# Kernel tuning notes

Measured on AMD Instinct MI355X. Metric: run time of the kernel, lower is better.

## Reference

```python
import jax, jax.numpy as jnp
import numpy as np

B, S, E, H = 2, 2048, 512, 8
DH = E // H
SCALE = DH ** -0.5
TEMPERATURE = 1.0
LN_EPS = 1e-5


def setup_inputs() -> dict:
    key = jax.random.key(0)
    ks = jax.random.split(key, 12)
    s = E ** -0.5
    return {
        "q": jax.random.normal(ks[0], (B, S, E), jnp.float32),
        "k": jax.random.normal(ks[1], (B, S, E), jnp.float32),
        "v": jax.random.normal(ks[2], (B, S, E), jnp.float32),
        "Wq": jax.random.normal(ks[3], (E, E), jnp.float32) * s,
        "bq": jnp.zeros((E,), jnp.float32),
        "Wk": jax.random.normal(ks[4], (E, E), jnp.float32) * s,
        "bk": jnp.zeros((E,), jnp.float32),
        "Wv": jax.random.normal(ks[5], (E, E), jnp.float32) * s,
        "bv": jnp.zeros((E,), jnp.float32),
        "Wo": jax.random.normal(ks[6], (E, E), jnp.float32) * s,
        "bo": jnp.zeros((E,), jnp.float32),
        "ln_g": jnp.ones((E,), jnp.float32),
        "ln_b": jnp.zeros((E,), jnp.float32),
    }


def reference(q, k, v, Wq, bq, Wk, bk, Wv, bv, Wo, bo, ln_g, ln_b):
    # QKV projections (nn.Linear: x @ W.T + b)
    qh = (q @ Wq.T + bq).reshape(B, S, H, DH).transpose(0, 2, 1, 3)  # [B,H,S,Dh]
    kh = (k @ Wk.T + bk).reshape(B, S, H, DH).transpose(0, 2, 1, 3)
    vh = (v @ Wv.T + bv).reshape(B, S, H, DH).transpose(0, 2, 1, 3)
    # attention scores [B,H,S,S], scaled then divided by temperature
    scores = jnp.einsum('bhqd,bhkd->bhqk', qh, kh) * (SCALE / TEMPERATURE)
    attn = jax.nn.softmax(scores, axis=-1)
    # dropout is identity in eval mode
    x = jnp.einsum('bhqk,bhkd->bhqd', attn, vh)  # [B,H,S,Dh]
    x = x.transpose(0, 2, 1, 3).reshape(B, S, E)
    # out projection + LayerNorm
    y = x @ Wo.T + bo
    mu = jnp.mean(y, axis=-1, keepdims=True)
    var = jnp.var(y, axis=-1, keepdims=True)
    out = (y - mu) * jax.lax.rsqrt(var + LN_EPS) * ln_g + ln_b
    return out
```

## Files before the change

kernel.cpp:

```cpp
#include <hip/hip_runtime.h>
#include <hip/hip_bf16.h>
#include <stdint.h>

#define B_ 2
#define S_ 2048
#define E_ 512
#define H_ 8
#define DH_ 64
#define BH_ (B_*H_)
#define M_ (B_*S_)

typedef short short8 __attribute__((ext_vector_type(8)));
typedef float f32x4 __attribute__((ext_vector_type(4)));
typedef float f32x16 __attribute__((ext_vector_type(16)));
typedef int int4v __attribute__((ext_vector_type(4)));

#define QSCALE 0.18033688011112042f

#if __has_builtin(__builtin_amdgcn_exp2f)
#define EXP2(x) __builtin_amdgcn_exp2f(x)
#else
#define EXP2(x) exp2f(x)
#endif

__device__ __forceinline__ float asf(uint32_t u) { return __builtin_bit_cast(float, u); }
__device__ __forceinline__ uint32_t asu(float f) { return __builtin_bit_cast(uint32_t, f); }

__device__ __forceinline__ ushort f2bf(float f) {
  uint32_t u = __builtin_bit_cast(uint32_t, f);
  u += 0x7fffu + ((u >> 16) & 1u);
  return (ushort)(u >> 16);
}

__device__ __forceinline__ uint32_t cvtpk(float lo, float hi) {
  uint32_t r;
  asm("v_cvt_pk_bf16_f32 %0, %1, %2" : "=v"(r) : "v"(lo), "v"(hi));
  return r;
}

__device__ __forceinline__ void swap32(uint32_t a, uint32_t b, uint32_t& o0, uint32_t& o1) {
#if __has_builtin(__builtin_amdgcn_permlane32_swap)
  typedef int v2i __attribute__((ext_vector_type(2)));
  v2i r = __builtin_amdgcn_permlane32_swap((int)a, (int)b, false, false);
  o0 = (uint32_t)r.x; o1 = (uint32_t)r.y;
#else
  int laneid = (int)(threadIdx.x & 63);
  uint32_t pa = (uint32_t)__shfl_xor((int)a, 32, 64);
  uint32_t pb = (uint32_t)__shfl_xor((int)b, 32, 64);
  bool hi = laneid >= 32;
  o0 = hi ? pb : a;
  o1 = hi ? b : pa;
#endif
}

__device__ __forceinline__ void gll16(const void* g, void* l) {
  __builtin_amdgcn_global_load_lds((const __attribute__((address_space(1))) void*)g,
                                   (__attribute__((address_space(3))) void*)l,
                                   16, 0, 0);
}

struct CvtArgs {
  const float* s[7];
  ushort* d[7];
  int nq[7];
};

__global__ __launch_bounds__(256) void cvt_kernel(CvtArgs a) {
  int seg = blockIdx.y;
  int i = blockIdx.x * 256 + threadIdx.x;
  if (i >= a.nq[seg]) return;
  float4 v = ((const float4*)a.s[seg])[i];
  ushort4 o;
  o.x = f2bf(v.x); o.y = f2bf(v.y); o.z = f2bf(v.z); o.w = f2bf(v.w);
  ((ushort4*)a.d[seg])[i] = o;
}

template<int EPI>
__global__ __launch_bounds__(256) void gemm_bt(
    const ushort* __restrict__ A0, const ushort* __restrict__ A1, const ushort* __restrict__ A2,
    const ushort* __restrict__ W0, const ushort* __restrict__ W1, const ushort* __restrict__ W2,
    const float* __restrict__ bias0, const float* __restrict__ bias1, const float* __restrict__ bias2,
    ushort* O0, ushort* O1, ushort* O2, float* Yout)
{
  const int K = E_;
  int z = blockIdx.z;
  const ushort* A = (z == 0) ? A0 : ((z == 1) ? A1 : A2);
  const ushort* W = (z == 0) ? W0 : ((z == 1) ? W1 : W2);
  const float* bias = (z == 0) ? bias0 : ((z == 1) ? bias1 : bias2);
  ushort* O = (z == 0) ? O0 : ((z == 1) ? O1 : O2);
  float scale = (EPI == 0 && z == 0) ? QSCALE : 1.0f;

  int n0 = blockIdx.x * 128, m0 = blockIdx.y * 128;
  int tid = threadIdx.x, lane = tid & 63, wid = tid >> 6;
  int wm = wid >> 1, wn = wid & 1;

  __shared__ ushort As[128 * 32];
  __shared__ ushort Bs[128 * 32];

  f32x4 acc[4][4];
#pragma unroll
  for (int i = 0; i < 4; ++i)
#pragma unroll
    for (int j = 0; j < 4; ++j)
      acc[i][j] = (f32x4){0.f, 0.f, 0.f, 0.f};

  for (int kt = 0; kt < K / 32; ++kt) {
    int k0 = kt * 32;
#pragma unroll
    for (int c = 0; c < 2; ++c) {
      int f = c * 256 + tid;
      int r = f >> 2;
      int lc = (f & 3) ^ ((r >> 1) & 3);
      gll16(A + (m0 + r) * K + k0 + lc * 8, (char*)As + (c * 256 + wid * 64) * 16);
    }
#pragma unroll
    for (int c = 0; c < 2; ++c) {
      int f = c * 256 + tid;
      int r = f >> 2;
      int lc = (f & 3) ^ ((r >> 1) & 3);
      gll16(W + (n0 + r) * K + k0 + lc * 8, (char*)Bs + (c * 256 + wid * 64) * 16);
    }
    __syncthreads();

    short8 af[4], bf[4];
#pragma unroll
    for (int fm = 0; fm < 4; ++fm) {
      int r = wm * 64 + fm * 16 + (lane & 15);
      int phys = (lane >> 4) ^ ((r >> 1) & 3);
      af[fm] = *(const short8*)((const char*)As + r * 64 + phys * 16);
    }
#pragma unroll
    for (int fn = 0; fn < 4; ++fn) {
      int r = wn * 64 + fn * 16 + (lane & 15);
      int phys = (lane >> 4) ^ ((r >> 1) & 3);
      bf[fn] = *(const short8*)((const char*)Bs + r * 64 + phys * 16);
    }
#pragma unroll
    for (int fm = 0; fm < 4; ++fm)
#pragma unroll
      for (int fn = 0; fn < 4; ++fn)
        acc[fm][fn] = __builtin_amdgcn_mfma_f32_16x16x32_bf16(af[fm], bf[fn], acc[fm][fn], 0, 0, 0);
    __syncthreads();
  }

#pragma unroll
  for (int fm = 0; fm < 4; ++fm) {
#pragma unroll
    for (int fn = 0; fn < 4; ++fn) {
#pragma unroll
      for (int j = 0; j < 4; ++j) {
        int m = m0 + wm * 64 + fm * 16 + (lane >> 4) * 4 + j;
        int n = n0 + wn * 64 + fn * 16 + (lane & 15);
        float v = (acc[fm][fn][j] + bias[n]) * scale;
        if constexpr (EPI == 0) {
          int b = m >> 11, s = m & (S_ - 1);
          int h = n >> 6, d = n & 63;
          O[((b * H_ + h) * S_ + s) * DH_ + d] = f2bf(v);
        } else {
          Yout[m * E_ + n] = v;
        }
      }
    }
  }
}

__global__ __launch_bounds__(256) void vtrans(const ushort* __restrict__ Vh, ushort* __restrict__ Vt) {
  int bh = blockIdx.y;
  int s0 = blockIdx.x * 64;
  __shared__ ushort t[64][72];
  int tid = threadIdx.x;
  const ushort* src = Vh + ((size_t)bh * S_ + s0) * DH_;
  int r = tid >> 2, c0 = (tid & 3) * 16;
#pragma unroll
  for (int i = 0; i < 2; ++i) {
    short8 v = *(const short8*)(src + r * DH_ + c0 + i * 8);
#pragma unroll
    for (int kx = 0; kx < 8; ++kx) t[r][c0 + i * 8 + kx] = (ushort)v[kx];
  }
  __syncthreads();
  int d = tid >> 2, j0 = (tid & 3) * 16;
  ushort* dst = Vt + ((size_t)bh * DH_ + d) * S_ + s0 + j0;
#pragma unroll
  for (int i = 0; i < 2; ++i) {
    short8 o;
#pragma unroll
    for (int kx = 0; kx < 8; ++kx) o[kx] = (short)t[j0 + i * 8 + kx][d];
    *(short8*)(dst + i * 8) = o;
  }
}

__global__ __launch_bounds__(256, 4) void attn_kernel(const ushort* __restrict__ Qh,
                                                      const ushort* __restrict__ Kh,
                                                      const ushort* __restrict__ Vt,
                                                      ushort* __restrict__ X) {
  int bh = blockIdx.x;
  int q0 = blockIdx.y * 64;
  int tid = threadIdx.x, lane = tid & 63, wid = tid >> 6;
  int wq = wid & 1, wk = wid >> 1;
  int hi = lane >> 5;

  __shared__ ushort lds_[16384];
  char* L = (char*)lds_;

  const ushort* Kg = Kh + (size_t)bh * S_ * DH_;
  const ushort* Vg = Vt + (size_t)bh * DH_ * S_;

  int q = q0 + wq * 32 + (lane & 31);
  const ushort* Qrow = Qh + ((size_t)bh * S_ + q) * DH_;
  short8 qf[4];
#pragma unroll
  for (int ds = 0; ds < 4; ++ds)
    qf[ds] = *(const short8*)(Qrow + ds * 16 + hi * 8);

  f32x16 sacc, oacc[2];
#pragma unroll
  for (int r = 0; r < 16; ++r) { oacc[0][r] = 0.f; oacc[1][r] = 0.f; }
  float m_r = -INFINITY, l_r = 0.f;

  const int NT = 32;

#define STAGE(buf, t)                                                          \
  do {                                                                         \
    _Pragma("unroll")                                                          \
    for (int w2 = 0; w2 < 2; ++w2) {                                           \
      int kb = w2 * 1024 + (t) * 32;                                           \
      char* Kd = L + (buf) * 16384 + w2 * 8192;                                \
      char* Vd = Kd + 4096;                                                    \
      {                                                                        \
        int r = tid >> 3, lc = (tid & 7) ^ (r & 7);                            \
        gll16(Kg + (size_t)(kb + r) * DH_ + lc * 8, Kd + wid * 1024);          \
      }                                                                        \
      {                                                                        \
        int rho = tid >> 3, l2 = (tid & 7) ^ (rho & 7);                        \
        int d = rho + ((l2 >> 2) << 5), kc = (l2 & 3) * 8;                     \
        gll16(Vg + (size_t)d * S_ + kb + kc, Vd + wid * 1024);                 \
      }                                                                        \
    }                                                                          \
  } while (0)

  STAGE(0, 0);
  __syncthreads();

  for (int t = 0; t < NT; ++t) {
    int cur = t & 1;
    if (t + 1 < NT) STAGE(cur ^ 1, t + 1);

    const char* Kt = L + cur * 16384 + wk * 8192;
    const char* Vtile = Kt + 4096;

#pragma unroll
    for (int r = 0; r < 16; ++r) sacc[r] = 0.f;
    int kl = lane & 31;
#pragma unroll
    for (int ds = 0; ds < 4; ++ds) {
      short8 kf = *(const short8*)(Kt + kl * 128 + (((2 * ds + hi) ^ (kl & 7)) * 16));
      sacc = __builtin_amdgcn_mfma_f32_32x32x16_bf16(kf, qf[ds], sacc, 0, 0, 0);
    }

    float mx = fmaxf(fmaxf(sacc[0], sacc[1]), sacc[2]);
    mx = fmaxf(mx, fmaxf(fmaxf(sacc[3], sacc[4]), sacc[5]));
    mx = fmaxf(mx, fmaxf(fmaxf(sacc[6], sacc[7]), sacc[8]));
    mx = fmaxf(mx, fmaxf(fmaxf(sacc[9], sacc[10]), sacc[11]));
    mx = fmaxf(mx, fmaxf(fmaxf(sacc[12], sacc[13]), sacc[14]));
    mx = fmaxf(mx, sacc[15]);
    bool skip = __all(mx - m_r <= 8.0f);
    if (!skip) {
      uint32_t e0, e1;
      swap32(asu(mx), asu(mx), e0, e1);
      float mnew = fmaxf(m_r, fmaxf(asf(e0), asf(e1)));
      float scf = EXP2(m_r - mnew);
      m_r = mnew;
      l_r *= scf;
#pragma unroll
      for (int dblk = 0; dblk < 2; ++dblk)
#pragma unroll
        for (int r = 0; r < 16; ++r) oacc[dblk][r] *= scf;
    }
    float rs0 = 0.f, rs1 = 0.f;
#pragma unroll
    for (int r = 0; r < 16; r += 2) {
      float p0 = EXP2(sacc[r] - m_r);
      float p1 = EXP2(sacc[r + 1] - m_r);
      sacc[r] = p0; sacc[r + 1] = p1;
      rs0 += p0; rs1 += p1;
    }
    float rs = rs0 + rs1;
    {
      uint32_t e0, e1;
      swap32(asu(rs), asu(rs), e0, e1);
      l_r += asf(e0) + asf(e1);
    }

    uint32_t w[8];
#pragma unroll
    for (int i = 0; i < 8; ++i)
      w[i] = cvtpk(sacc[2 * i], sacc[2 * i + 1]);

    short8 pf[2];
#pragma unroll
    for (int ks = 0; ks < 2; ++ks) {
      uint32_t e01, e45, e23, e67;
      swap32(w[4 * ks + 0], w[4 * ks + 2], e01, e45);
      swap32(w[4 * ks + 1], w[4 * ks + 3], e23, e67);
      int4v iv;
      iv[0] = (int)e01; iv[1] = (int)e23; iv[2] = (int)e45; iv[3] = (int)e67;
      pf[ks] = __builtin_bit_cast(short8, iv);
    }

#pragma unroll
    for (int ks = 0; ks < 2; ++ks) {
      int rho = lane & 31;
#pragma unroll
      for (int dblk = 0; dblk < 2; ++dblk) {
        int lch = dblk * 4 + 2 * ks + hi;
        short8 vf = *(const short8*)(Vtile + rho * 128 + ((lch ^ (rho & 7)) * 16));
        oacc[dblk] = __builtin_amdgcn_mfma_f32_32x32x16_bf16(vf, pf[ks], oacc[dblk], 0, 0, 0);
      }
    }

    __syncthreads();
  }
#undef STAGE

  float* fl = (float*)L;
  if (wk == 1) {
#pragma unroll
    for (int dblk = 0; dblk < 2; ++dblk)
#pragma unroll
      for (int r = 0; r < 16; ++r)
        fl[((wq * 2 + dblk) * 16 + r) * 64 + lane] = oacc[dblk][r];
    fl[4096 + wq * 64 + lane] = m_r;
    fl[4224 + wq * 64 + lane] = l_r;
  }
  __syncthreads();
  if (wk == 0) {
    float m1 = fl[4096 + wq * 64 + lane];
    float l1 = fl[4224 + wq * 64 + lane];
    float mstar = fmaxf(m_r, m1);
    float a0 = EXP2(m_r - mstar);
    float a1 = EXP2(m1 - mstar);
    float lstar = l_r * a0 + l1 * a1;
    float invl = 1.0f / lstar;
    int b = bh >> 3, h = bh & 7;
    int s = q0 + wq * 32 + (lane & 31);
    ushort* Xrow = X + (size_t)(b * S_ + s) * E_ + h * DH_;
#pragma unroll
    for (int dblk = 0; dblk < 2; ++dblk) {
#pragma unroll
      for (int i = 0; i < 8; ++i) {
        int r0 = 2 * i, r1 = 2 * i + 1;
        float o0 = (oacc[dblk][r0] * a0 + fl[((wq * 2 + dblk) * 16 + r0) * 64 + lane] * a1) * invl;
        float o1 = (oacc[dblk][r1] * a0 + fl[((wq * 2 + dblk) * 16 + r1) * 64 + lane] * a1) * invl;
        int d = dblk * 32 + (r0 & 3) + 8 * (r0 >> 2) + 4 * hi;
        *(uint32_t*)(Xrow + d) = cvtpk(o0, o1);
      }
    }
  }
}

__global__ __launch_bounds__(256) void ln_kernel(const float* __restrict__ Y,
                                                 const float* __restrict__ g,
                                                 const float* __restrict__ bta,
                                                 float* __restrict__ out) {
  int tid = threadIdx.x, lane = tid & 63, wid = tid >> 6;
  int row = blockIdx.x * 4 + wid;
  const float* y = Y + (size_t)row * E_;
  float4 v0 = *(const float4*)(y + lane * 8);
  float4 v1 = *(const float4*)(y + lane * 8 + 4);
  float s = v0.x + v0.y + v0.z + v0.w + v1.x + v1.y + v1.z + v1.w;
  float q = v0.x * v0.x + v0.y * v0.y + v0.z * v0.z + v0.w * v0.w +
            v1.x * v1.x + v1.y * v1.y + v1.z * v1.z + v1.w * v1.w;
#pragma unroll
  for (int msk = 1; msk < 64; msk <<= 1) {
    s += __shfl_xor(s, msk);
    q += __shfl_xor(q, msk);
  }
  float mu = s * (1.f / E_);
  float var = q * (1.f / E_) - mu * mu;
  float inv = rsqrtf(var + 1e-5f);
  float4 g0 = *(const float4*)(g + lane * 8);
  float4 g1 = *(const float4*)(g + lane * 8 + 4);
  float4 b0 = *(const float4*)(bta + lane * 8);
  float4 b1 = *(const float4*)(bta + lane * 8 + 4);
  float4 o0, o1;
  o0.x = (v0.x - mu) * inv * g0.x + b0.x;
  o0.y = (v0.y - mu) * inv * g0.y + b0.y;
  o0.z = (v0.z - mu) * inv * g0.z + b0.z;
  o0.w = (v0.w - mu) * inv * g0.w + b0.w;
  o1.x = (v1.x - mu) * inv * g1.x + b1.x;
  o1.y = (v1.y - mu) * inv * g1.y + b1.y;
  o1.z = (v1.z - mu) * inv * g1.z + b1.z;
  o1.w = (v1.w - mu) * inv * g1.w + b1.w;
  float* op = out + (size_t)row * E_;
  *(float4*)(op + lane * 8) = o0;
  *(float4*)(op + lane * 8 + 4) = o1;
}

extern "C" void kernel_launch(void* const* d_in, const int* in_sizes, int n_in,
                              void* d_out, int out_size, void* d_ws, size_t ws_size,
                              hipStream_t stream) {
  const float* q = (const float*)d_in[0];
  const float* k = (const float*)d_in[1];
  const float* v = (const float*)d_in[2];
  const float* Wq = (const float*)d_in[3];
  const float* bq = (const float*)d_in[4];
  const float* Wk = (const float*)d_in[5];
  const float* bk = (const float*)d_in[6];
  const float* Wv = (const float*)d_in[7];
  const float* bv = (const float*)d_in[8];
  const float* Wo = (const float*)d_in[9];
  const float* bo = (const float*)d_in[10];
  const float* ln_g = (const float*)d_in[11];
  const float* ln_b = (const float*)d_in[12];

  char* ws = (char*)d_ws;
  const size_t MB = 1024 * 1024;
  ushort* qb  = (ushort*)(ws + 0 * MB);
  ushort* kb  = (ushort*)(ws + 4 * MB);
  ushort* vb  = (ushort*)(ws + 8 * MB);
  ushort* Wqb = (ushort*)(ws + 12 * MB);
  ushort* Wkb = (ushort*)(ws + 12 * MB + 512 * 1024);
  ushort* Wvb = (ushort*)(ws + 13 * MB);
  ushort* Wob = (ushort*)(ws + 13 * MB + 512 * 1024);
  ushort* Qhb = (ushort*)(ws + 14 * MB);
  ushort* Khb = (ushort*)(ws + 18 * MB);
  ushort* Vhb = (ushort*)(ws + 22 * MB);
  ushort* Vtb = (ushort*)(ws + 26 * MB);
  ushort* Xb  = (ushort*)(ws + 30 * MB);
  float*  Yb  = (float*)(ws + 34 * MB);

  CvtArgs ca;
  ca.s[0] = q;  ca.d[0] = qb;  ca.nq[0] = (B_ * S_ * E_) / 4;
  ca.s[1] = k;  ca.d[1] = kb;  ca.nq[1] = (B_ * S_ * E_) / 4;
  ca.s[2] = v;  ca.d[2] = vb;  ca.nq[2] = (B_ * S_ * E_) / 4;
  ca.s[3] = Wq; ca.d[3] = Wqb; ca.nq[3] = (E_ * E_) / 4;
  ca.s[4] = Wk; ca.d[4] = Wkb; ca.nq[4] = (E_ * E_) / 4;
  ca.s[5] = Wv; ca.d[5] = Wvb; ca.nq[5] = (E_ * E_) / 4;
  ca.s[6] = Wo; ca.d[6] = Wob; ca.nq[6] = (E_ * E_) / 4;

  cvt_kernel<<<dim3(2048, 7), dim3(256), 0, stream>>>(ca);

  gemm_bt<0><<<dim3(4, 32, 3), dim3(256), 0, stream>>>(
      qb, kb, vb, Wqb, Wkb, Wvb, bq, bk, bv, Qhb, Khb, Vhb, (float*)nullptr);

  vtrans<<<dim3(S_ / 64, BH_), dim3(256), 0, stream>>>(Vhb, Vtb);

  attn_kernel<<<dim3(BH_, S_ / 64), dim3(256), 0, stream>>>(Qhb, Khb, Vtb, Xb);

  gemm_bt<1><<<dim3(4, 32, 1), dim3(256), 0, stream>>>(
      Xb, Xb, Xb, Wob, Wob, Wob, bo, bo, bo,
      (ushort*)nullptr, (ushort*)nullptr, (ushort*)nullptr, Yb);

  ln_kernel<<<dim3(M_ / 4), dim3(256), 0, stream>>>(Yb, ln_g, ln_b, (float*)d_out);
}
```

Before: 77.65 us.

## Double-buffer GEMM LDS tiles and raise wave priority around attention MFMAs

The projection GEMM now keeps two LDS buffers for the A and W tiles and issues the global-to-LDS loads for the next k-step before computing on the current one. This drops one barrier per iteration and is meant to hide load latency behind the MFMAs. It doubles the GEMM's LDS use, which can lower occupancy. The attention kernel also wraps its QK and PV MFMA blocks in s_setprio so waves in their matrix phase get scheduling priority over waves doing softmax work.

```diff
diff --git a/kernel.cpp b/kernel.cpp
--- a/kernel.cpp
+++ b/kernel.cpp
@@ -83,6 +83,7 @@
     ushort* O0, ushort* O1, ushort* O2, float* Yout)
 {
   const int K = E_;
+  const int NKT = K / 32;
   int z = blockIdx.z;
   const ushort* A = (z == 0) ? A0 : ((z == 1) ? A1 : A2);
   const ushort* W = (z == 0) ? W0 : ((z == 1) ? W1 : W2);
@@ -94,8 +95,8 @@
   int tid = threadIdx.x, lane = tid & 63, wid = tid >> 6;
   int wm = wid >> 1, wn = wid & 1;
 
-  __shared__ ushort As[128 * 32];
-  __shared__ ushort Bs[128 * 32];
+  __shared__ ushort As[2][128 * 32];
+  __shared__ ushort Bs[2][128 * 32];
 
   f32x4 acc[4][4];
 #pragma unroll
@@ -104,44 +105,50 @@
     for (int j = 0; j < 4; ++j)
       acc[i][j] = (f32x4){0.f, 0.f, 0.f, 0.f};
 
-  for (int kt = 0; kt < K / 32; ++kt) {
-    int k0 = kt * 32;
-#pragma unroll
-    for (int c = 0; c < 2; ++c) {
-      int f = c * 256 + tid;
-      int r = f >> 2;
-      int lc = (f & 3) ^ ((r >> 1) & 3);
-      gll16(A + (m0 + r) * K + k0 + lc * 8, (char*)As + (c * 256 + wid * 64) * 16);
-    }
-#pragma unroll
-    for (int c = 0; c < 2; ++c) {
-      int f = c * 256 + tid;
-      int r = f >> 2;
-      int lc = (f & 3) ^ ((r >> 1) & 3);
-      gll16(W + (n0 + r) * K + k0 + lc * 8, (char*)Bs + (c * 256 + wid * 64) * 16);
-    }
-    __syncthreads();
+#define GSTAGE(buf, kt)                                                        \
+  do {                                                                         \
+    int k0 = (kt) * 32;                                                        \
+    _Pragma("unroll")                                                          \
+    for (int c = 0; c < 2; ++c) {                                              \
+      int f = c * 256 + tid;                                                   \
+      int r = f >> 2;                                                          \
+      int lc = (f & 3) ^ ((r >> 1) & 3);                                       \
+      gll16(A + (m0 + r) * K + k0 + lc * 8,                                    \
+            (char*)As[buf] + (c * 256 + wid * 64) * 16);                       \
+      gll16(W + (n0 + r) * K + k0 + lc * 8,                                    \
+            (char*)Bs[buf] + (c * 256 + wid * 64) * 16);                       \
+    }                                                                          \
+  } while (0)
+
+  GSTAGE(0, 0);
+  __syncthreads();
+
+  for (int kt = 0; kt < NKT; ++kt) {
+    int cur = kt & 1;
+    if (kt + 1 < NKT) GSTAGE(cur ^ 1, kt + 1);
 
     short8 af[4], bf[4];
 #pragma unroll
     for (int fm = 0; fm < 4; ++fm) {
       int r = wm * 64 + fm * 16 + (lane & 15);
       int phys = (lane >> 4) ^ ((r >> 1) & 3);
-      af[fm] = *(const short8*)((const char*)As + r * 64 + phys * 16);
+      af[fm] = *(const short8*)((const char*)As[cur] + r * 64 + phys * 16);
     }
 #pragma unroll
     for (int fn = 0; fn < 4; ++fn) {
       int r = wn * 64 + fn * 16 + (lane & 15);
       int phys = (lane >> 4) ^ ((r >> 1) & 3);
-      bf[fn] = *(const short8*)((const char*)Bs + r * 64 + phys * 16);
+      bf[fn] = *(const short8*)((const char*)Bs[cur] + r * 64 + phys * 16);
     }
 #pragma unroll
     for (int fm = 0; fm < 4; ++fm)
 #pragma unroll
       for (int fn = 0; fn < 4; ++fn)
         acc[fm][fn] = __builtin_amdgcn_mfma_f32_16x16x32_bf16(af[fm], bf[fn], acc[fm][fn], 0, 0, 0);
+
     __syncthreads();
   }
+#undef GSTAGE
 
 #pragma unroll
   for (int fm = 0; fm < 4; ++fm) {
@@ -251,11 +258,13 @@
 #pragma unroll
     for (int r = 0; r < 16; ++r) sacc[r] = 0.f;
     int kl = lane & 31;
+    __builtin_amdgcn_s_setprio(1);
 #pragma unroll
     for (int ds = 0; ds < 4; ++ds) {
       short8 kf = *(const short8*)(Kt + kl * 128 + (((2 * ds + hi) ^ (kl & 7)) * 16));
       sacc = __builtin_amdgcn_mfma_f32_32x32x16_bf16(kf, qf[ds], sacc, 0, 0, 0);
     }
+    __builtin_amdgcn_s_setprio(0);
 
     float mx = fmaxf(fmaxf(sacc[0], sacc[1]), sacc[2]);
     mx = fmaxf(mx, fmaxf(fmaxf(sacc[3], sacc[4]), sacc[5]));
@@ -307,6 +316,7 @@
       pf[ks] = __builtin_bit_cast(short8, iv);
     }
 
+    __builtin_amdgcn_s_setprio(1);
 #pragma unroll
     for (int ks = 0; ks < 2; ++ks) {
       int rho = lane & 31;
@@ -317,6 +327,7 @@
         oacc[dblk] = __builtin_amdgcn_mfma_f32_32x32x16_bf16(vf, pf[ks], oacc[dblk], 0, 0, 0);
       }
     }
+    __builtin_amdgcn_s_setprio(0);
 
     __syncthreads();
   }
```

Result: no change. 78.44 us (+1.0%).
